# Kernel optimization log

Measured on AMD Instinct MI355X. Metric: run time of the kernel, lower is better.

Reference implementation:

```python
import jax, jax.numpy as jnp
import numpy as np

EPS = 1e-7
B, F, C, H, W, D = 2, 2, 64, 32, 104, 96


def _pix_homog(h, w):
    ys, xs = jnp.meshgrid(jnp.arange(h, dtype=jnp.float32),
                          jnp.arange(w, dtype=jnp.float32), indexing='ij')
    return jnp.stack([xs.ravel(), ys.ravel(), jnp.ones(h * w, jnp.float32)], 0)  # [3, H*W]


def setup_inputs() -> dict:
    key = jax.random.key(0)
    k1, k2 = jax.random.split(key)
    current_feats = jax.random.normal(k1, (B, C, H, W), jnp.float32)
    lookup_feats = jax.random.normal(k2, (B, F, C, H, W), jnp.float32)

    rng = np.random.RandomState(0)
    # intrinsics at matching (feature) resolution, monodepth2-style
    Km = np.eye(4, dtype=np.float32)
    Km[0, 0] = 0.58 * W
    Km[1, 1] = 1.92 * H
    Km[0, 2] = 0.5 * W
    Km[1, 2] = 0.5 * H
    K = np.tile(Km[None], (B, 1, 1))
    invK = np.linalg.inv(K).astype(np.float32)

    # near-identity relative poses (small rotation perturbation + small translation)
    poses = np.tile(np.eye(4, dtype=np.float32)[None, None], (B, F, 1, 1))
    poses[:, :, :3, :3] += 0.02 * rng.randn(B, F, 3, 3).astype(np.float32)
    poses[:, :, :3, 3] = 0.1 * rng.randn(B, F, 3).astype(np.float32)

    depth_bins = jnp.linspace(0.1, 20.0, D, dtype=jnp.float32)
    return {
        'current_feats': current_feats,
        'lookup_feats': lookup_feats,
        'poses': jnp.asarray(poses),
        'K': jnp.asarray(K),
        'invK': jnp.asarray(invK),
        'depth_bins': depth_bins,
    }


def _grid_sample_zeros(lfT, gx, gy, h, w):
    """Bilinear grid_sample, align_corners=True, padding_mode='zeros'.
    lfT: [B,F,H,W,C]; gx,gy: [B,F,D,H,W] in pixel coords. -> [B,F,D,H,W,C]"""
    x0 = jnp.floor(gx)
    y0 = jnp.floor(gy)
    x0i = x0.astype(jnp.int32)
    y0i = y0.astype(jnp.int32)
    wx1 = gx - x0
    wy1 = gy - y0
    wx0 = 1.0 - wx1
    wy0 = 1.0 - wy1
    bb = jnp.arange(lfT.shape[0])[:, None, None, None, None]
    ff = jnp.arange(lfT.shape[1])[None, :, None, None, None]

    def corner(yi, xi, wgt):
        m = ((xi >= 0) & (xi < w) & (yi >= 0) & (yi < h)).astype(lfT.dtype)
        xc = jnp.clip(xi, 0, w - 1)
        yc = jnp.clip(yi, 0, h - 1)
        v = lfT[bb, ff, yc, xc]                      # [B,F,D,H,W,C]
        return v * (m * wgt)[..., None]

    return (corner(y0i, x0i, wy0 * wx0) + corner(y0i, x0i + 1, wy0 * wx1)
            + corner(y0i + 1, x0i, wy1 * wx0) + corner(y0i + 1, x0i + 1, wy1 * wx1))


def reference(current_feats, lookup_feats, poses, K, invK, depth_bins):
    b, c, h, w = current_feats.shape
    f = lookup_feats.shape[1]
    d = depth_bins.shape[0]

    # Backproject: world points for each hypothesised depth plane
    pix = _pix_homog(h, w)                                   # [3, HW]
    cam = jnp.einsum('bij,jn->bin', invK[:, :3, :3], pix)    # [B,3,HW]
    pts = depth_bins[None, :, None, None] * cam[:, None]     # [B,D,3,HW]
    world = jnp.concatenate([pts, jnp.ones((b, d, 1, h * w), pts.dtype)], 2)  # [B,D,4,HW]

    # Project into each lookup frame
    P = jnp.einsum('bij,bfjk->bfik', K, poses)[:, :, :3, :]  # [B,F,3,4]
    cpts = jnp.einsum('bfij,bdjn->bfdin', P, world)          # [B,F,D,3,HW]
    xy = cpts[:, :, :, :2] / (cpts[:, :, :, 2:3] + EPS)      # pixel coords [B,F,D,2,HW]
    xy = xy.reshape(b, f, d, 2, h, w)
    gx, gy = xy[:, :, :, 0], xy[:, :, :, 1]                  # [B,F,D,H,W]

    # edge mask (detach in original -> stop_gradient)
    sx, sy = jax.lax.stop_gradient(gx), jax.lax.stop_gradient(gy)
    edge = ((sx >= 2.0) & (sx <= w - 2) & (sy >= 2.0) & (sy <= h - 2)).astype(jnp.float32)
    interior = jnp.zeros((h, w), jnp.float32).at[2:-2, 2:-2].set(1.0)
    edge_mask = edge * interior                               # [B,F,D,H,W]

    # warp lookup features and L1-diff against current features
    lfT = lookup_feats.transpose(0, 1, 3, 4, 2)               # [B,F,H,W,C]
    warped = _grid_sample_zeros(lfT, gx, gy, h, w)            # [B,F,D,H,W,C]
    cur = current_feats.transpose(0, 2, 3, 1)                 # [B,H,W,C]
    diffs = jnp.abs(warped - cur[:, None, None]).mean(-1) * edge_mask  # [B,F,D,H,W]

    # skip lookup frames whose pose is all-zero
    valid = (poses.sum((-2, -1)) != 0).astype(jnp.float32)    # [B,F]
    diffs = diffs * valid[:, :, None, None, None]

    cost = diffs.sum(1)                                        # [B,D,H,W]
    counts = (diffs > 0).astype(jnp.float32).sum(1)
    cost = cost / (counts + EPS)

    # set missing values to per-pixel max over depth bins
    missing = (cost == 0.0)
    cmax = cost.max(1, keepdims=True)
    cost = jnp.where(missing, cmax, cost)
    return cost
```

## Files before the change

### kernel.cpp

```cpp
#include <hip/hip_runtime.h>
#include <math.h>

constexpr int B_ = 2, F_ = 2, C_ = 64, H_ = 32, W_ = 104, D_ = 96;
constexpr int HW_ = H_ * W_;
#define EPSF 1e-7f

constexpr size_t LFT_OFF  = 0;
constexpr size_t CURT_OFF = LFT_OFF + (size_t)B_ * F_ * HW_ * C_;

constexpr int NT_BLKS = (HW_ / 32) * (C_ / 32) * (B_ * F_ + B_);

__global__ __launch_bounds__(256) void prep_kernel(
        const float* __restrict__ cur, const float* __restrict__ lf,
        float* __restrict__ ws) {
    __shared__ float tile[32][33];
    int bid = blockIdx.x;
    int slice = bid / 208;
    int rem   = bid % 208;
    int nb = rem % 104, cb = rem / 104;
    const float* inS;
    float* outS;
    if (slice < B_ * F_) {
        inS  = lf + (size_t)slice * C_ * HW_;
        outS = ws + LFT_OFF + (size_t)slice * HW_ * C_;
    } else {
        int s2 = slice - B_ * F_;
        inS  = cur + (size_t)s2 * C_ * HW_;
        outS = ws + CURT_OFF + (size_t)s2 * HW_ * C_;
    }
    int t = threadIdx.x;
    int tx = t & 31, ty = t >> 5;
    int n0 = nb * 32, c0 = cb * 32;
    #pragma unroll
    for (int k = 0; k < 32; k += 8)
        tile[ty + k][tx] = inS[(size_t)(c0 + ty + k) * HW_ + n0 + tx];
    __syncthreads();
    #pragma unroll
    for (int k = 0; k < 32; k += 8)
        outS[(size_t)(n0 + ty + k) * C_ + c0 + tx] = tile[tx][ty + k];
}

__global__ __launch_bounds__(256) void mega_kernel(
        const float* __restrict__ poses, const float* __restrict__ K,
        const float* __restrict__ invK, const float* __restrict__ depth_bins,
        const float* __restrict__ ws, float* __restrict__ out) {
    int t   = threadIdx.x;
    int bid = blockIdx.x;
    int xt  = bid % 13;  int r = bid / 13;
    int y   = r % H_;
    int b   = r / H_;

    if (y < 2 || y >= H_ - 2) {
        for (int k = t; k < 8 * D_; k += 256) {
            int d = k >> 3, px = k & 7;
            out[((size_t)(b * D_ + d) * H_ + y) * W_ + xt * 8 + px] = 0.0f;
        }
        return;
    }

    __shared__ int   offs[F_][D_][8];
    __shared__ float wts [F_][D_][8][4];
    __shared__ float costb[8][D_];
    __shared__ float pmax[32][8];
    __shared__ float cmaxb[8];

    #pragma unroll
    for (int f = 0; f < F_; ++f) {
        const float* Kb   = K + (size_t)b * 16;
        const float* pose = poses + (size_t)(b * F_ + f) * 16;
        float P[12];
        #pragma unroll
        for (int i = 0; i < 3; ++i) {
            #pragma unroll
            for (int k = 0; k < 4; ++k) {
                float acc = __fmul_rn(Kb[i*4+0], pose[0*4+k]);
                acc = __fmaf_rn(Kb[i*4+1], pose[1*4+k], acc);
                acc = __fmaf_rn(Kb[i*4+2], pose[2*4+k], acc);
                acc = __fmaf_rn(Kb[i*4+3], pose[3*4+k], acc);
                P[i*4+k] = acc;
            }
        }
        float vs = 0.f;
        #pragma unroll
        for (int j = 0; j < 16; ++j) vs += pose[j];
        bool valid = (vs != 0.f);
        const float* iK = invK + (size_t)b * 16;

        #pragma unroll
        for (int k = 0; k < 3; ++k) {
            int idx = t + 256 * k;
            int dd = idx >> 3, px = idx & 7;
            int x = xt * 8 + px;
            float xf = (float)x, yf = (float)y;
            float cam0 = __fmul_rn(iK[0], xf); cam0 = __fmaf_rn(iK[1], yf, cam0); cam0 = __fmaf_rn(iK[2],  1.0f, cam0);
            float cam1 = __fmul_rn(iK[4], xf); cam1 = __fmaf_rn(iK[5], yf, cam1); cam1 = __fmaf_rn(iK[6],  1.0f, cam1);
            float cam2 = __fmul_rn(iK[8], xf); cam2 = __fmaf_rn(iK[9], yf, cam2); cam2 = __fmaf_rn(iK[10], 1.0f, cam2);
            float depth = depth_bins[dd];
            float p0 = __fmul_rn(depth, cam0);
            float p1 = __fmul_rn(depth, cam1);
            float p2 = __fmul_rn(depth, cam2);
            float c0 = __fmul_rn(P[0], p0); c0 = __fmaf_rn(P[1], p1, c0); c0 = __fmaf_rn(P[2],  p2, c0); c0 = __fmaf_rn(P[3],  1.0f, c0);
            float c1 = __fmul_rn(P[4], p0); c1 = __fmaf_rn(P[5], p1, c1); c1 = __fmaf_rn(P[6],  p2, c1); c1 = __fmaf_rn(P[7],  1.0f, c1);
            float c2 = __fmul_rn(P[8], p0); c2 = __fmaf_rn(P[9], p1, c2); c2 = __fmaf_rn(P[10], p2, c2); c2 = __fmaf_rn(P[11], 1.0f, c2);
            float denom = __fadd_rn(c2, EPSF);
            float gx = c0 / denom;
            float gy = c1 / denom;
            bool interior = (x >= 2) && (x <= W_ - 3);
            bool m = valid && interior && (gx >= 2.0f) && (gx <= (float)(W_ - 2))
                                       && (gy >= 2.0f) && (gy <= (float)(H_ - 2));
            if (m) {
                float x0f = floorf(gx), y0f = floorf(gy);
                int   x0  = (int)x0f,   y0  = (int)y0f;
                float wx1 = gx - x0f, wy1 = gy - y0f;
                float wx0 = 1.f - wx1, wy0 = 1.f - wy1;
                wts[f][dd][px][0] = wy0 * wx0;
                wts[f][dd][px][1] = wy0 * wx1;
                wts[f][dd][px][2] = wy1 * wx0;
                wts[f][dd][px][3] = wy1 * wx1;
                offs[f][dd][px] = (y0 * W_ + x0) * C_;
            } else {
                offs[f][dd][px] = -1;
                wts[f][dd][px][0] = 0.f;
                wts[f][dd][px][1] = 0.f;
                wts[f][dd][px][2] = 0.f;
                wts[f][dd][px][3] = 0.f;
            }
        }
    }
    __syncthreads();

    {
        int lane = t & 15, px = (t >> 4) & 7, half = t >> 7;
        int x = xt * 8 + px;
        const float4 cv = *(const float4*)(ws + CURT_OFF
                            + ((size_t)((b * H_ + y) * W_ + x)) * C_ + lane * 4);
        const float* lfb[F_];
        lfb[0] = ws + LFT_OFF + (size_t)(b * F_ + 0) * HW_ * C_ + lane * 4;
        lfb[1] = ws + LFT_OFF + (size_t)(b * F_ + 1) * HW_ * C_ + lane * 4;

        float4 cc[F_][4];
        int oprev[F_] = { -1, -1 };
        #pragma unroll
        for (int f = 0; f < F_; ++f)
            cc[f][0] = cc[f][1] = cc[f][2] = cc[f][3] = make_float4(0.f, 0.f, 0.f, 0.f);

        int dbeg = half * (D_ / 2), dend = dbeg + (D_ / 2);
        for (int dc = dbeg; dc < dend; ++dc) {
            float costsum = 0.f, counts = 0.f;
            #pragma unroll
            for (int f = 0; f < F_; ++f) {
                int  o = offs[f][dc][px];
                bool m = (o >= 0);
                if (m && o != oprev[f]) {
                    const float* bp = lfb[f] + o;
                    cc[f][0] = *(const float4*)(bp);
                    cc[f][1] = *(const float4*)(bp + C_);
                    cc[f][2] = *(const float4*)(bp + W_ * C_);
                    cc[f][3] = *(const float4*)(bp + W_ * C_ + C_);
                    oprev[f] = o;
                }
                float w00 = wts[f][dc][px][0];
                float w01 = wts[f][dc][px][1];
                float w10 = wts[f][dc][px][2];
                float w11 = wts[f][dc][px][3];
                float s;
                s  = fabsf(cc[f][0].x*w00 + cc[f][1].x*w01 + cc[f][2].x*w10 + cc[f][3].x*w11 - cv.x);
                s += fabsf(cc[f][0].y*w00 + cc[f][1].y*w01 + cc[f][2].y*w10 + cc[f][3].y*w11 - cv.y);
                s += fabsf(cc[f][0].z*w00 + cc[f][1].z*w01 + cc[f][2].z*w10 + cc[f][3].z*w11 - cv.z);
                s += fabsf(cc[f][0].w*w00 + cc[f][1].w*w01 + cc[f][2].w*w10 + cc[f][3].w*w11 - cv.w);
                s += __shfl_xor(s, 1);
                s += __shfl_xor(s, 2);
                s += __shfl_xor(s, 4);
                s += __shfl_xor(s, 8);
                float diff = __fmul_rn(s, 1.0f / 64.0f) * (m ? 1.0f : 0.0f);
                costsum += diff;
                counts  += (diff > 0.f) ? 1.0f : 0.0f;
            }
            float cost = costsum / __fadd_rn(counts, EPSF);
            if (lane == 0) costb[px][dc] = cost;
        }
    }
    __syncthreads();

    {
        int j = t >> 3, px = t & 7;
        float v[3];
        float pm = 0.f;
        #pragma unroll
        for (int k = 0; k < 3; ++k) {
            v[k] = costb[px][j + 32 * k];
            pm = fmaxf(pm, v[k]);
        }
        pmax[j][px] = pm;
        __syncthreads();
        if (t < 8) {
            float cm = 0.f;
            #pragma unroll
            for (int jj = 0; jj < 32; ++jj) cm = fmaxf(cm, pmax[jj][t]);
            cmaxb[t] = cm;
        }
        __syncthreads();
        float cm = cmaxb[px];
        int x = xt * 8 + px;
        #pragma unroll
        for (int k = 0; k < 3; ++k) {
            int d = j + 32 * k;
            out[((size_t)(b * D_ + d) * H_ + y) * W_ + x] = (v[k] == 0.0f) ? cm : v[k];
        }
    }
}

extern "C" void kernel_launch(void* const* d_in, const int* in_sizes, int n_in,
                              void* d_out, int out_size, void* d_ws, size_t ws_size,
                              hipStream_t stream) {
    const float* cur        = (const float*)d_in[0];
    const float* lf         = (const float*)d_in[1];
    const float* poses      = (const float*)d_in[2];
    const float* K          = (const float*)d_in[3];
    const float* invK       = (const float*)d_in[4];
    const float* depth_bins = (const float*)d_in[5];
    float* out = (float*)d_out;
    float* ws  = (float*)d_ws;

    prep_kernel<<<NT_BLKS, 256, 0, stream>>>(cur, lf, ws);
    mega_kernel<<<B_ * H_ * 13, 256, 0, stream>>>(poses, K, invK, depth_bins, ws, out);
}
```

Measured before the change: 109.8 us.

## Use 512-thread blocks splitting depth into quarters with padded px-major shared layout

The cost-volume kernel now launches 512 threads per block, so each thread group handles a quarter of the depth bins instead of half. This shortens the serial gather loop and doubles the waves in flight for this small grid. The per-pixel sample offsets and weights move to a px-major, padded shared-memory layout with float4 weights, and the next bin's offset and weights are loaded one iteration ahead. The frame loop is also hand-unrolled. The costs are a larger block that may limit residency per CU, and idle threads during the final max reduction.

```diff
diff --git a/kernel.cpp b/kernel.cpp
--- a/kernel.cpp
+++ b/kernel.cpp
@@ -9,6 +9,8 @@
 constexpr size_t CURT_OFF = LFT_OFF + (size_t)B_ * F_ * HW_ * C_;
 
 constexpr int NT_BLKS = (HW_ / 32) * (C_ / 32) * (B_ * F_ + B_);
+constexpr int DPAD  = D_ + 1;
+constexpr int DPADI = D_ + 4;
 
 __global__ __launch_bounds__(256) void prep_kernel(
         const float* __restrict__ cur, const float* __restrict__ lf,
@@ -40,7 +42,7 @@
         outS[(size_t)(n0 + ty + k) * C_ + c0 + tx] = tile[tx][ty + k];
 }
 
-__global__ __launch_bounds__(256) void mega_kernel(
+__global__ __launch_bounds__(512, 4) void mega_kernel(
         const float* __restrict__ poses, const float* __restrict__ K,
         const float* __restrict__ invK, const float* __restrict__ depth_bins,
         const float* __restrict__ ws, float* __restrict__ out) {
@@ -51,18 +53,18 @@
     int b   = r / H_;
 
     if (y < 2 || y >= H_ - 2) {
-        for (int k = t; k < 8 * D_; k += 256) {
+        for (int k = t; k < 8 * D_; k += 512) {
             int d = k >> 3, px = k & 7;
             out[((size_t)(b * D_ + d) * H_ + y) * W_ + xt * 8 + px] = 0.0f;
         }
         return;
     }
 
-    __shared__ int   offs[F_][D_][8];
-    __shared__ float wts [F_][D_][8][4];
-    __shared__ float costb[8][D_];
-    __shared__ float pmax[32][8];
-    __shared__ float cmaxb[8];
+    __shared__ int    offsL[F_][8][DPADI];
+    __shared__ float4 wtsL [F_][8][DPAD];
+    __shared__ float  costb[8][DPAD];
+    __shared__ float  pmax[32][8];
+    __shared__ float  cmaxb[8];
 
     #pragma unroll
     for (int f = 0; f < F_; ++f) {
@@ -87,43 +89,40 @@
         const float* iK = invK + (size_t)b * 16;
 
         #pragma unroll
-        for (int k = 0; k < 3; ++k) {
-            int idx = t + 256 * k;
-            int dd = idx >> 3, px = idx & 7;
-            int x = xt * 8 + px;
-            float xf = (float)x, yf = (float)y;
-            float cam0 = __fmul_rn(iK[0], xf); cam0 = __fmaf_rn(iK[1], yf, cam0); cam0 = __fmaf_rn(iK[2],  1.0f, cam0);
-            float cam1 = __fmul_rn(iK[4], xf); cam1 = __fmaf_rn(iK[5], yf, cam1); cam1 = __fmaf_rn(iK[6],  1.0f, cam1);
-            float cam2 = __fmul_rn(iK[8], xf); cam2 = __fmaf_rn(iK[9], yf, cam2); cam2 = __fmaf_rn(iK[10], 1.0f, cam2);
-            float depth = depth_bins[dd];
-            float p0 = __fmul_rn(depth, cam0);
-            float p1 = __fmul_rn(depth, cam1);
-            float p2 = __fmul_rn(depth, cam2);
-            float c0 = __fmul_rn(P[0], p0); c0 = __fmaf_rn(P[1], p1, c0); c0 = __fmaf_rn(P[2],  p2, c0); c0 = __fmaf_rn(P[3],  1.0f, c0);
-            float c1 = __fmul_rn(P[4], p0); c1 = __fmaf_rn(P[5], p1, c1); c1 = __fmaf_rn(P[6],  p2, c1); c1 = __fmaf_rn(P[7],  1.0f, c1);
-            float c2 = __fmul_rn(P[8], p0); c2 = __fmaf_rn(P[9], p1, c2); c2 = __fmaf_rn(P[10], p2, c2); c2 = __fmaf_rn(P[11], 1.0f, c2);
-            float denom = __fadd_rn(c2, EPSF);
-            float gx = c0 / denom;
-            float gy = c1 / denom;
-            bool interior = (x >= 2) && (x <= W_ - 3);
-            bool m = valid && interior && (gx >= 2.0f) && (gx <= (float)(W_ - 2))
-                                       && (gy >= 2.0f) && (gy <= (float)(H_ - 2));
-            if (m) {
-                float x0f = floorf(gx), y0f = floorf(gy);
-                int   x0  = (int)x0f,   y0  = (int)y0f;
-                float wx1 = gx - x0f, wy1 = gy - y0f;
-                float wx0 = 1.f - wx1, wy0 = 1.f - wy1;
-                wts[f][dd][px][0] = wy0 * wx0;
-                wts[f][dd][px][1] = wy0 * wx1;
-                wts[f][dd][px][2] = wy1 * wx0;
-                wts[f][dd][px][3] = wy1 * wx1;
-                offs[f][dd][px] = (y0 * W_ + x0) * C_;
-            } else {
-                offs[f][dd][px] = -1;
-                wts[f][dd][px][0] = 0.f;
-                wts[f][dd][px][1] = 0.f;
-                wts[f][dd][px][2] = 0.f;
-                wts[f][dd][px][3] = 0.f;
+        for (int k = 0; k < 2; ++k) {
+            int idx = t + 512 * k;
+            if (idx < 8 * D_) {
+                int dd = idx >> 3, px = idx & 7;
+                int x = xt * 8 + px;
+                float xf = (float)x, yf = (float)y;
+                float cam0 = __fmul_rn(iK[0], xf); cam0 = __fmaf_rn(iK[1], yf, cam0); cam0 = __fmaf_rn(iK[2],  1.0f, cam0);
+                float cam1 = __fmul_rn(iK[4], xf); cam1 = __fmaf_rn(iK[5], yf, cam1); cam1 = __fmaf_rn(iK[6],  1.0f, cam1);
+                float cam2 = __fmul_rn(iK[8], xf); cam2 = __fmaf_rn(iK[9], yf, cam2); cam2 = __fmaf_rn(iK[10], 1.0f, cam2);
+                float depth = depth_bins[dd];
+                float p0 = __fmul_rn(depth, cam0);
+                float p1 = __fmul_rn(depth, cam1);
+                float p2 = __fmul_rn(depth, cam2);
+                float c0 = __fmul_rn(P[0], p0); c0 = __fmaf_rn(P[1], p1, c0); c0 = __fmaf_rn(P[2],  p2, c0); c0 = __fmaf_rn(P[3],  1.0f, c0);
+                float c1 = __fmul_rn(P[4], p0); c1 = __fmaf_rn(P[5], p1, c1); c1 = __fmaf_rn(P[6],  p2, c1); c1 = __fmaf_rn(P[7],  1.0f, c1);
+                float c2 = __fmul_rn(P[8], p0); c2 = __fmaf_rn(P[9], p1, c2); c2 = __fmaf_rn(P[10], p2, c2); c2 = __fmaf_rn(P[11], 1.0f, c2);
+                float denom = __fadd_rn(c2, EPSF);
+                float gx = c0 / denom;
+                float gy = c1 / denom;
+                bool interior = (x >= 2) && (x <= W_ - 3);
+                bool m = valid && interior && (gx >= 2.0f) && (gx <= (float)(W_ - 2))
+                                           && (gy >= 2.0f) && (gy <= (float)(H_ - 2));
+                if (m) {
+                    float x0f = floorf(gx), y0f = floorf(gy);
+                    int   x0  = (int)x0f,   y0  = (int)y0f;
+                    float wx1 = gx - x0f, wy1 = gy - y0f;
+                    float wx0 = 1.f - wx1, wy0 = 1.f - wy1;
+                    wtsL[f][px][dd] = make_float4(wy0 * wx0, wy0 * wx1,
+                                                  wy1 * wx0, wy1 * wx1);
+                    offsL[f][px][dd] = (y0 * W_ + x0) * C_;
+                } else {
+                    offsL[f][px][dd] = -1;
+                    wtsL[f][px][dd] = make_float4(0.f, 0.f, 0.f, 0.f);
+                }
             }
         }
     }
@@ -134,40 +133,42 @@
         int x = xt * 8 + px;
         const float4 cv = *(const float4*)(ws + CURT_OFF
                             + ((size_t)((b * H_ + y) * W_ + x)) * C_ + lane * 4);
-        const float* lfb[F_];
-        lfb[0] = ws + LFT_OFF + (size_t)(b * F_ + 0) * HW_ * C_ + lane * 4;
-        lfb[1] = ws + LFT_OFF + (size_t)(b * F_ + 1) * HW_ * C_ + lane * 4;
-
-        float4 cc[F_][4];
-        int oprev[F_] = { -1, -1 };
-        #pragma unroll
-        for (int f = 0; f < F_; ++f)
-            cc[f][0] = cc[f][1] = cc[f][2] = cc[f][3] = make_float4(0.f, 0.f, 0.f, 0.f);
-
-        int dbeg = half * (D_ / 2), dend = dbeg + (D_ / 2);
+        const float* lf0 = ws + LFT_OFF + (size_t)(b * F_ + 0) * HW_ * C_ + lane * 4;
+        const float* lf1 = ws + LFT_OFF + (size_t)(b * F_ + 1) * HW_ * C_ + lane * 4;
+
+        float4 cc0[4], cc1[4];
+        int oprev0 = -1, oprev1 = -1;
+        #pragma unroll
+        for (int k = 0; k < 4; ++k)
+            cc0[k] = cc1[k] = make_float4(0.f, 0.f, 0.f, 0.f);
+
+        int dbeg = half * (D_ / 4), dend = dbeg + (D_ / 4);
+        int    on0 = offsL[0][px][dbeg], on1 = offsL[1][px][dbeg];
+        float4 wn0 = wtsL[0][px][dbeg],  wn1 = wtsL[1][px][dbeg];
+
         for (int dc = dbeg; dc < dend; ++dc) {
+            int    oc0 = on0, oc1 = on1;
+            float4 wc0 = wn0, wc1 = wn1;
+            int nx = (dc + 1 < dend) ? dc + 1 : dc;
+            on0 = offsL[0][px][nx]; wn0 = wtsL[0][px][nx];
+            on1 = offsL[1][px][nx]; wn1 = wtsL[1][px][nx];
+
             float costsum = 0.f, counts = 0.f;
-            #pragma unroll
-            for (int f = 0; f < F_; ++f) {
-                int  o = offs[f][dc][px];
-                bool m = (o >= 0);
-                if (m && o != oprev[f]) {
-                    const float* bp = lfb[f] + o;
-                    cc[f][0] = *(const float4*)(bp);
-                    cc[f][1] = *(const float4*)(bp + C_);
-                    cc[f][2] = *(const float4*)(bp + W_ * C_);
-                    cc[f][3] = *(const float4*)(bp + W_ * C_ + C_);
-                    oprev[f] = o;
+            {
+                bool m = (oc0 >= 0);
+                if (m && oc0 != oprev0) {
+                    const float* bp = lf0 + oc0;
+                    cc0[0] = *(const float4*)(bp);
+                    cc0[1] = *(const float4*)(bp + C_);
+                    cc0[2] = *(const float4*)(bp + W_ * C_);
+                    cc0[3] = *(const float4*)(bp + W_ * C_ + C_);
+                    oprev0 = oc0;
                 }
-                float w00 = wts[f][dc][px][0];
-                float w01 = wts[f][dc][px][1];
-                float w10 = wts[f][dc][px][2];
-                float w11 = wts[f][dc][px][3];
                 float s;
-                s  = fabsf(cc[f][0].x*w00 + cc[f][1].x*w01 + cc[f][2].x*w10 + cc[f][3].x*w11 - cv.x);
-                s += fabsf(cc[f][0].y*w00 + cc[f][1].y*w01 + cc[f][2].y*w10 + cc[f][3].y*w11 - cv.y);
-                s += fabsf(cc[f][0].z*w00 + cc[f][1].z*w01 + cc[f][2].z*w10 + cc[f][3].z*w11 - cv.z);
-                s += fabsf(cc[f][0].w*w00 + cc[f][1].w*w01 + cc[f][2].w*w10 + cc[f][3].w*w11 - cv.w);
+                s  = fabsf(cc0[0].x*wc0.x + cc0[1].x*wc0.y + cc0[2].x*wc0.z + cc0[3].x*wc0.w - cv.x);
+                s += fabsf(cc0[0].y*wc0.x + cc0[1].y*wc0.y + cc0[2].y*wc0.z + cc0[3].y*wc0.w - cv.y);
+                s += fabsf(cc0[0].z*wc0.x + cc0[1].z*wc0.y + cc0[2].z*wc0.z + cc0[3].z*wc0.w - cv.z);
+                s += fabsf(cc0[0].w*wc0.x + cc0[1].w*wc0.y + cc0[2].w*wc0.z + cc0[3].w*wc0.w - cv.w);
                 s += __shfl_xor(s, 1);
                 s += __shfl_xor(s, 2);
                 s += __shfl_xor(s, 4);
@@ -176,6 +177,29 @@
                 costsum += diff;
                 counts  += (diff > 0.f) ? 1.0f : 0.0f;
             }
+            {
+                bool m = (oc1 >= 0);
+                if (m && oc1 != oprev1) {
+                    const float* bp = lf1 + oc1;
+                    cc1[0] = *(const float4*)(bp);
+                    cc1[1] = *(const float4*)(bp + C_);
+                    cc1[2] = *(const float4*)(bp + W_ * C_);
+                    cc1[3] = *(const float4*)(bp + W_ * C_ + C_);
+                    oprev1 = oc1;
+                }
+                float s;
+                s  = fabsf(cc1[0].x*wc1.x + cc1[1].x*wc1.y + cc1[2].x*wc1.z + cc1[3].x*wc1.w - cv.x);
+                s += fabsf(cc1[0].y*wc1.x + cc1[1].y*wc1.y + cc1[2].y*wc1.z + cc1[3].y*wc1.w - cv.y);
+                s += fabsf(cc1[0].z*wc1.x + cc1[1].z*wc1.y + cc1[2].z*wc1.z + cc1[3].z*wc1.w - cv.z);
+                s += fabsf(cc1[0].w*wc1.x + cc1[1].w*wc1.y + cc1[2].w*wc1.z + cc1[3].w*wc1.w - cv.w);
+                s += __shfl_xor(s, 1);
+                s += __shfl_xor(s, 2);
+                s += __shfl_xor(s, 4);
+                s += __shfl_xor(s, 8);
+                float diff = __fmul_rn(s, 1.0f / 64.0f) * (m ? 1.0f : 0.0f);
+                costsum += diff;
+                counts  += (diff > 0.f) ? 1.0f : 0.0f;
+            }
             float cost = costsum / __fadd_rn(counts, EPSF);
             if (lane == 0) costb[px][dc] = cost;
         }
@@ -185,13 +209,15 @@
     {
         int j = t >> 3, px = t & 7;
         float v[3];
-        float pm = 0.f;
-        #pragma unroll
-        for (int k = 0; k < 3; ++k) {
-            v[k] = costb[px][j + 32 * k];
-            pm = fmaxf(pm, v[k]);
-        }
-        pmax[j][px] = pm;
+        if (t < 256) {
+            float pm = 0.f;
+            #pragma unroll
+            for (int k = 0; k < 3; ++k) {
+                v[k] = costb[px][j + 32 * k];
+                pm = fmaxf(pm, v[k]);
+            }
+            pmax[j][px] = pm;
+        }
         __syncthreads();
         if (t < 8) {
             float cm = 0.f;
@@ -200,12 +226,14 @@
             cmaxb[t] = cm;
         }
         __syncthreads();
-        float cm = cmaxb[px];
-        int x = xt * 8 + px;
-        #pragma unroll
-        for (int k = 0; k < 3; ++k) {
-            int d = j + 32 * k;
-            out[((size_t)(b * D_ + d) * H_ + y) * W_ + x] = (v[k] == 0.0f) ? cm : v[k];
+        if (t < 256) {
+            float cm = cmaxb[px];
+            int x = xt * 8 + px;
+            #pragma unroll
+            for (int k = 0; k < 3; ++k) {
+                int d = j + 32 * k;
+                out[((size_t)(b * D_ + d) * H_ + y) * W_ + x] = (v[k] == 0.0f) ? cm : v[k];
+            }
         }
     }
 }
@@ -223,5 +251,5 @@
     float* ws  = (float*)d_ws;
 
     prep_kernel<<<NT_BLKS, 256, 0, stream>>>(cur, lf, ws);
-    mega_kernel<<<B_ * H_ * 13, 256, 0, stream>>>(poses, K, invK, depth_bins, ws, out);
+    mega_kernel<<<B_ * H_ * 13, 512, 0, stream>>>(poses, K, invK, depth_bins, ws, out);
 }
```

Result: no change. 110.5 us (+0.6%).
